# Optimization experiments

Hardware: AMD Instinct MI355X
Metric: run time of the kernel (lower is better)

Reference implementation:

```python
import jax, jax.numpy as jnp
import numpy as np

N, D, H, B, E = 100000, 256, 256, 128, 128
STEPS = 5


def setup_inputs() -> dict:
    key = jax.random.key(0)
    ks = jax.random.split(key, 16)
    w = lambda i, shape: (jax.random.normal(ks[i], shape, jnp.float32) * 0.05)
    inp = {
        "x": jax.random.normal(ks[0], (N, D), jnp.float32),
        "batch_idxs": jnp.sort(jax.random.randint(ks[1], (N,), 0, B)),
        # FNN: Linear(D,H) -> ELU -> Linear(H,H)
        "fnn_W1": w(2, (D, H)), "fnn_b1": jnp.zeros((H,), jnp.float32),
        "fnn_W2": w(3, (H, H)), "fnn_b2": jnp.zeros((H,), jnp.float32),
        # 3-layer LSTM, input 2H (layer 0) / H (layers 1,2), hidden H
        "Wih0": w(4, (4 * H, 2 * H)), "Whh0": w(5, (4 * H, H)),
        "bih0": jnp.zeros((4 * H,), jnp.float32), "bhh0": jnp.zeros((4 * H,), jnp.float32),
        "Wih1": w(6, (4 * H, H)), "Whh1": w(7, (4 * H, H)),
        "bih1": jnp.zeros((4 * H,), jnp.float32), "bhh1": jnp.zeros((4 * H,), jnp.float32),
        "Wih2": w(8, (4 * H, H)), "Whh2": w(9, (4 * H, H)),
        "bih2": jnp.zeros((4 * H,), jnp.float32), "bhh2": jnp.zeros((4 * H,), jnp.float32),
        # output Linear(2H, E)
        "out_W": w(10, (2 * H, E)), "out_b": jnp.zeros((E,), jnp.float32),
    }
    return inp


def _lstm_cell(xin, h, c, Wih, Whh, bih, bhh):
    gates = xin @ Wih.T + bih + h @ Whh.T + bhh  # (B, 4H)
    i, f, g, o = jnp.split(gates, 4, axis=-1)    # PyTorch gate order i,f,g,o
    c = jax.nn.sigmoid(f) * c + jax.nn.sigmoid(i) * jnp.tanh(g)
    h = jax.nn.sigmoid(o) * jnp.tanh(c)
    return h, c


def reference(x, batch_idxs, fnn_W1, fnn_b1, fnn_W2, fnn_b2,
              Wih0, Whh0, bih0, bhh0, Wih1, Whh1, bih1, bhh1,
              Wih2, Whh2, bih2, bhh2, out_W, out_b):
    # FNN (ELU between layers)
    hfeat = jax.nn.elu(x @ fnn_W1 + fnn_b1) @ fnn_W2 + fnn_b2  # (N, H)

    Wihs, Whhs = (Wih0, Wih1, Wih2), (Whh0, Whh1, Whh2)
    bihs, bhhs = (bih0, bih1, bih2), (bhh0, bhh1, bhh2)
    hs = [jnp.zeros((B, H), hfeat.dtype) for _ in range(3)]
    cs = [jnp.zeros((B, H), hfeat.dtype) for _ in range(3)]
    q_star = jnp.zeros((B, 2 * H), hfeat.dtype)

    for _ in range(STEPS):
        layer_in = q_star
        for l in range(3):
            hs[l], cs[l] = _lstm_cell(layer_in, hs[l], cs[l], Wihs[l], Whhs[l], bihs[l], bhhs[l])
            layer_in = hs[l]
        q = layer_in  # (B, H)
        # segment (per-graph) attention softmax over nodes
        e = jnp.sum(hfeat * q[batch_idxs], axis=-1)                     # (N,)
        m = jax.ops.segment_max(e, batch_idxs, num_segments=B)
        m = jnp.where(jnp.isfinite(m), m, 0.0)                          # guard empty segments
        ex = jnp.exp(e - m[batch_idxs])
        denom = jax.ops.segment_sum(ex, batch_idxs, num_segments=B) + 1e-16
        a = ex / denom[batch_idxs]                                      # (N,)
        r = jax.ops.segment_sum(a[:, None] * hfeat, batch_idxs, num_segments=B)  # (B, H)
        q_star = jnp.concatenate([q, r], axis=-1)                       # (B, 2H)

    return q_star @ out_W + out_b  # (B, E)
```

## Files before the change

kernel.cpp:

```cpp
#include <hip/hip_runtime.h>

#define NN 100000
#define NSTEP 5
#define LSTR 264

typedef unsigned short ushort_t;
typedef __attribute__((ext_vector_type(8))) short short8;
typedef __attribute__((ext_vector_type(4))) float floatx4;

__device__ __forceinline__ ushort_t f2bf(float f){
  union { float f; unsigned u; } v; v.f = f;
  unsigned r = v.u + 0x7fffu + ((v.u >> 16) & 1u);
  return (ushort_t)(r >> 16);
}
__device__ __forceinline__ float bf2f(ushort_t s){
  union { unsigned u; float f; } v; v.u = ((unsigned)s) << 16;
  return v.f;
}
__device__ __forceinline__ float sigf(float x){ return 1.0f/(1.0f+__expf(-x)); }

__global__ __launch_bounds__(512, 2) void fnn_fused(const float* __restrict__ x,
    const ushort_t* __restrict__ W1P, const float* __restrict__ b1,
    const ushort_t* __restrict__ W2P, const float* __restrict__ b2,
    ushort_t* __restrict__ hfeat)
{
  __shared__ ushort_t xbuf[2][32 * LSTR];
  __shared__ ushort_t tbuf[32 * LSTR];
  int tid = threadIdx.x;
  int w = tid >> 6, lane = tid & 63, qd = lane >> 4, r16 = lane & 15;

  short8 w1r[8][2], w2r[8][2];
  #pragma unroll
  for (int kc = 0; kc < 8; kc++)
    #pragma unroll
    for (int j = 0; j < 2; j++){
      size_t off = (size_t)(((w*2 + j)*8 + kc)*64 + lane)*8;
      w1r[kc][j] = *(const short8*)(W1P + off);
      w2r[kc][j] = *(const short8*)(W2P + off);
    }
  float bb1[2], bb2[2];
  #pragma unroll
  for (int j = 0; j < 2; j++){
    int col = w*32 + j*16 + r16;
    bb1[j] = b1[col];
    bb2[j] = b2[col];
  }

  size_t row0 = (size_t)blockIdx.x * 160;

  float4 xv[4];
  #pragma unroll
  for (int it = 0; it < 4; it++){
    int idx = it*512 + tid;
    xv[it] = *(const float4*)(x + (row0 + (idx>>6))*256 + (idx&63)*4);
  }
  #pragma unroll
  for (int it = 0; it < 4; it++){
    int idx = it*512 + tid;
    ushort4 pk = make_ushort4(f2bf(xv[it].x), f2bf(xv[it].y), f2bf(xv[it].z), f2bf(xv[it].w));
    *(ushort4*)&xbuf[0][(idx>>6)*LSTR + (idx&63)*4] = pk;
  }
  __syncthreads();

  int cur = 0;
  for (int t = 0; t < 5; t++){
    size_t rowt = row0 + t*32;
    if (t < 4){
      #pragma unroll
      for (int it = 0; it < 4; it++){
        int idx = it*512 + tid;
        xv[it] = *(const float4*)(x + (rowt + 32 + (idx>>6))*256 + (idx&63)*4);
      }
    }

    floatx4 acc[2][2];
    #pragma unroll
    for (int i=0;i<2;i++)
      #pragma unroll
      for (int j=0;j<2;j++) acc[i][j] = (floatx4){0.f,0.f,0.f,0.f};
    #pragma unroll
    for (int kc = 0; kc < 8; kc++){
      short8 af[2];
      #pragma unroll
      for (int i=0;i<2;i++)
        af[i] = *(const short8*)&xbuf[cur][(i*16 + r16)*LSTR + kc*32 + qd*8];
      #pragma unroll
      for (int i=0;i<2;i++)
        #pragma unroll
        for (int j=0;j<2;j++)
          acc[i][j] = __builtin_amdgcn_mfma_f32_16x16x32_bf16(af[i], w1r[kc][j], acc[i][j], 0, 0, 0);
    }

    #pragma unroll
    for (int i=0;i<2;i++){
      #pragma unroll
      for (int j=0;j<2;j++){
        int col = w*32 + j*16 + r16;
        #pragma unroll
        for (int rr=0;rr<4;rr++){
          int row = i*16 + qd*4 + rr;
          float v = acc[i][j][rr] + bb1[j];
          v = v > 0.f ? v : (__expf(v) - 1.0f);
          tbuf[row * LSTR + col] = f2bf(v);
        }
      }
    }
    __syncthreads();

    #pragma unroll
    for (int i=0;i<2;i++)
      #pragma unroll
      for (int j=0;j<2;j++) acc[i][j] = (floatx4){0.f,0.f,0.f,0.f};
    #pragma unroll
    for (int kc = 0; kc < 8; kc++){
      short8 af[2];
      #pragma unroll
      for (int i=0;i<2;i++)
        af[i] = *(const short8*)&tbuf[(i*16 + r16)*LSTR + kc*32 + qd*8];
      #pragma unroll
      for (int i=0;i<2;i++)
        #pragma unroll
        for (int j=0;j<2;j++)
          acc[i][j] = __builtin_amdgcn_mfma_f32_16x16x32_bf16(af[i], w2r[kc][j], acc[i][j], 0, 0, 0);
    }

    #pragma unroll
    for (int i=0;i<2;i++){
      #pragma unroll
      for (int j=0;j<2;j++){
        int col = w*32 + j*16 + r16;
        #pragma unroll
        for (int rr=0;rr<4;rr++){
          size_t row = rowt + i*16 + qd*4 + rr;
          hfeat[row * 256 + col] = f2bf(acc[i][j][rr] + bb2[j]);
        }
      }
    }

    if (t < 4){
      #pragma unroll
      for (int it = 0; it < 4; it++){
        int idx = it*512 + tid;
        ushort4 pk = make_ushort4(f2bf(xv[it].x), f2bf(xv[it].y), f2bf(xv[it].z), f2bf(xv[it].w));
        *(ushort4*)&xbuf[cur^1][(idx>>6)*LSTR + (idx&63)*4] = pk;
      }
    }
    __syncthreads();
    cur ^= 1;
  }
}

__global__ __launch_bounds__(256) void lstm_layer(const ushort_t* __restrict__ A, int lda,
    const ushort_t* __restrict__ WcP, const float* __restrict__ bcp, int KC,
    float* __restrict__ c, ushort_t* __restrict__ dstA, int sA,
    ushort_t* __restrict__ dstB, int sB, float* __restrict__ qdst)
{
  __shared__ float sbuf[3][4][256];
  int tid = threadIdx.x, w = tid >> 6, lane = tid & 63, qd = lane >> 4, r16 = lane & 15;
  int m0 = (blockIdx.x & 7) * 16, nt = blockIdx.x >> 3;
  int kcq = KC >> 2;
  int kc0 = w * kcq;

  floatx4 acc[4];
  #pragma unroll
  for (int g=0; g<4; g++) acc[g] = (floatx4){0.f,0.f,0.f,0.f};

  const ushort_t* Ar = A + (size_t)(m0 + r16) * lda + qd * 8;
  for (int kc = kc0; kc < kc0 + kcq; kc++){
    short8 av = *(const short8*)(Ar + kc*32);
    #pragma unroll
    for (int g = 0; g < 4; g++){
      short8 bv = *(const short8*)(WcP + (size_t)((((g*16 + nt)*KC) + kc)*64 + lane)*8);
      acc[g] = __builtin_amdgcn_mfma_f32_16x16x32_bf16(av, bv, acc[g], 0, 0, 0);
    }
  }
  if (w){
    #pragma unroll
    for (int g=0; g<4; g++) *(floatx4*)&sbuf[w-1][g][lane*4] = acc[g];
  }
  __syncthreads();
  if (w == 0){
    #pragma unroll
    for (int g=0; g<4; g++)
      #pragma unroll
      for (int t=0; t<3; t++){
        floatx4 p = *(floatx4*)&sbuf[t][g][lane*4];
        acc[g] = acc[g] + p;
      }
    int h = nt*16 + r16;
    float bci = bcp[h], bcf = bcp[256+h], bcg = bcp[512+h], bco = bcp[768+h];
    #pragma unroll
    for (int rr=0; rr<4; rr++){
      int row = m0 + qd*4 + rr;
      float gi = acc[0][rr] + bci;
      float gf = acc[1][rr] + bcf;
      float gg = acc[2][rr] + bcg;
      float go = acc[3][rr] + bco;
      float cp = c[row*256 + h];
      float cn = sigf(gf)*cp + sigf(gi)*tanhf(gg);
      float hn = sigf(go)*tanhf(cn);
      c[row*256 + h] = cn;
      ushort_t hb = f2bf(hn);
      dstA[row*sA + h] = hb;
      dstB[row*sB + h] = hb;
      if (qdst) qdst[row*512 + h] = hn;
    }
  }
}

__global__ __launch_bounds__(256) void attn_onepass(const ushort_t* __restrict__ hfeat,
    const int* __restrict__ seg, const float* __restrict__ q_star,
    float* __restrict__ r_part, float* __restrict__ z_part)
{
  __shared__ float sred[4][260];
  int b = blockIdx.x >> 3, p = blockIdx.x & 7;
  int w = threadIdx.x >> 6, lane = threadIdx.x & 63;
  int s0 = seg[b], s1 = seg[b+1], len = s1 - s0;
  int q0 = s0 + ((len * p) >> 3);
  int q1 = s0 + ((len * (p+1)) >> 3);

  float S0=0.f, S1=0.f, S2=0.f, S3=0.f, Z=0.f;

  int n = q0 + w;
  if (n < q1){
    float4 q = *(const float4*)(q_star + (size_t)b*512 + lane*4);
    #define LOADH(nn) (*(const ushort4*)(hfeat + (size_t)(nn)*256 + lane*4))
    ushort4 ha = LOADH(n);
    ushort4 hb = ha;
    if (n + 4 < q1) hb = LOADH(n + 4);
    for (; n < q1; n += 8){
      ushort4 hc = ha, hd = hb;
      if (n + 8  < q1) hc = LOADH(n + 8);
      if (n + 12 < q1) hd = LOADH(n + 12);
      float a0=bf2f(ha.x), a1=bf2f(ha.y), a2=bf2f(ha.z), a3=bf2f(ha.w);
      float da = a0*q.x + a1*q.y + a2*q.z + a3*q.w;
      float b0=0.f,b1=0.f,b2=0.f,b3=0.f, db=0.f;
      int vB = (n + 4) < q1;
      if (vB){
        b0=bf2f(hb.x); b1=bf2f(hb.y); b2=bf2f(hb.z); b3=bf2f(hb.w);
        db = b0*q.x + b1*q.y + b2*q.z + b3*q.w;
      }
      #pragma unroll
      for (int off = 32; off; off >>= 1){
        da += __shfl_xor(da, off);
        db += __shfl_xor(db, off);
      }
      float wa = __expf(da);
      Z += wa; S0 += wa*a0; S1 += wa*a1; S2 += wa*a2; S3 += wa*a3;
      if (vB){
        float wb = __expf(db);
        Z += wb; S0 += wb*b0; S1 += wb*b1; S2 += wb*b2; S3 += wb*b3;
      }
      ha = hc; hb = hd;
    }
    #undef LOADH
  }

  *(float4*)&sred[w][lane*4] = (float4){S0, S1, S2, S3};
  if (lane == 0) sred[w][256] = Z;
  __syncthreads();
  int f = threadIdx.x;
  if (f < 256){
    float v = sred[0][f] + sred[1][f] + sred[2][f] + sred[3][f];
    r_part[((size_t)p*128 + b)*256 + f] = v;
    if (f == 0)
      z_part[p*128 + b] = sred[0][256] + sred[1][256] + sred[2][256] + sred[3][256];
  }
}

__global__ __launch_bounds__(256) void attn_fin(const float* __restrict__ r_part,
    const float* __restrict__ z_part, float* __restrict__ q_star, ushort_t* __restrict__ xc0,
    const float* __restrict__ outW, const float* __restrict__ outb,
    float* __restrict__ out, int last)
{
  __shared__ float qs[512];
  int b = blockIdx.x, f = threadIdx.x;
  float s = 0.f, z = 0.f;
  #pragma unroll
  for (int t = 0; t < 8; t++){
    s += r_part[((size_t)(t*128 + b))*256 + f];
    z += z_part[t*128 + b];
  }
  float v = s / (z + 1e-16f);
  q_star[b*512 + 256 + f] = v;
  xc0[b*768 + 256 + f] = f2bf(v);
  if (last){
    qs[f] = q_star[b*512 + f];
    qs[256 + f] = v;
    __syncthreads();
    if (f < 128){
      float acc = outb[f];
      for (int k = 0; k < 512; k++) acc += qs[k] * outW[k*128 + f];
      out[b*128 + f] = acc;
    }
  }
}

__global__ void prep_all(const float* __restrict__ W1, const float* __restrict__ W2,
    const float* __restrict__ Wih0, const float* __restrict__ Whh0,
    const float* __restrict__ Wih1, const float* __restrict__ Whh1,
    const float* __restrict__ Wih2, const float* __restrict__ Whh2,
    const float* __restrict__ bih0, const float* __restrict__ bhh0,
    const float* __restrict__ bih1, const float* __restrict__ bhh1,
    const float* __restrict__ bih2, const float* __restrict__ bhh2,
    const int* __restrict__ bidx,
    ushort_t* __restrict__ W1P, ushort_t* __restrict__ W2P,
    ushort_t* __restrict__ Wc0P, ushort_t* __restrict__ Wc1P, ushort_t* __restrict__ Wc2P,
    float* __restrict__ c, ushort_t* __restrict__ xc, float* __restrict__ q_star,
    float* __restrict__ bc, int* __restrict__ seg)
{
  int i = blockIdx.x*256 + threadIdx.x;
  if (i < 131072){
    const float* W = (i < 65536) ? W1 : W2;
    ushort_t* P = (i < 65536) ? W1P : W2P;
    int r = i & 65535;
    int T = r >> 12, r2 = r & 4095;
    int kc = r2 >> 9, l = (r2 >> 3) & 63, j = r2 & 7;
    int k = kc*32 + ((l>>4)<<3) + j;
    int n = T*16 + (l & 15);
    P[r] = f2bf(W[k*256 + n]);
    return;
  }
  i -= 131072;
  if (i < 786432){
    int T = i / 12288, r2 = i - T*12288;
    int kc = r2 >> 9, l = (r2 >> 3) & 63, j = r2 & 7;
    int k = kc*32 + ((l>>4)<<3) + j;
    int g = T >> 4, n = (T & 15)*16 + (l & 15);
    int row = g*256 + n;
    Wc0P[i] = f2bf(k < 512 ? Wih0[row*512 + k] : Whh0[row*256 + (k - 512)]);
    return;
  }
  i -= 786432;
  if (i < 1048576){
    const float* Wih = (i < 524288) ? Wih1 : Wih2;
    const float* Whh = (i < 524288) ? Whh1 : Whh2;
    ushort_t* P = (i < 524288) ? Wc1P : Wc2P;
    int r = i & 524287;
    int T = r >> 13, r2 = r & 8191;
    int kc = r2 >> 9, l = (r2 >> 3) & 63, j = r2 & 7;
    int k = kc*32 + ((l>>4)<<3) + j;
    int g = T >> 4, n = (T & 15)*16 + (l & 15);
    int row = g*256 + n;
    P[r] = f2bf(k < 256 ? Wih[row*256 + k] : Whh[row*256 + (k - 256)]);
    return;
  }
  i -= 1048576;
  if (i < 98304) { c[i] = 0.f; return; }
  i -= 98304;
  if (i < 229376) { xc[i] = 0; return; }
  i -= 229376;
  if (i < 65536) { q_star[i] = 0.f; return; }
  i -= 65536;
  if (i < 3072) {
    int l = i >> 10, g = i & 1023;
    const float* bi = (l == 0) ? bih0 : ((l == 1) ? bih1 : bih2);
    const float* bh = (l == 0) ? bhh0 : ((l == 1) ? bhh1 : bhh2);
    bc[i] = bi[g] + bh[g];
    return;
  }
  i -= 3072;
  if (i < 129) {
    int lo = 0, hi = NN;
    while (lo < hi){ int mid = (lo + hi) >> 1; if (bidx[mid] < i) lo = mid + 1; else hi = mid; }
    seg[i] = lo;
    return;
  }
}

extern "C" void kernel_launch(void* const* d_in, const int* in_sizes, int n_in,
                              void* d_out, int out_size, void* d_ws, size_t ws_size,
                              hipStream_t stream)
{
  const float* x    = (const float*)d_in[0];
  const int*   bidx = (const int*)  d_in[1];
  const float* W1   = (const float*)d_in[2];
  const float* b1   = (const float*)d_in[3];
  const float* W2   = (const float*)d_in[4];
  const float* b2   = (const float*)d_in[5];
  const float* Wih0 = (const float*)d_in[6];
  const float* Whh0 = (const float*)d_in[7];
  const float* bih0 = (const float*)d_in[8];
  const float* bhh0 = (const float*)d_in[9];
  const float* Wih1 = (const float*)d_in[10];
  const float* Whh1 = (const float*)d_in[11];
  const float* bih1 = (const float*)d_in[12];
  const float* bhh1 = (const float*)d_in[13];
  const float* Wih2 = (const float*)d_in[14];
  const float* Whh2 = (const float*)d_in[15];
  const float* bih2 = (const float*)d_in[16];
  const float* bhh2 = (const float*)d_in[17];
  const float* outW = (const float*)d_in[18];
  const float* outb = (const float*)d_in[19];

  char* p = (char*)d_ws;
  auto alloc = [&](size_t bytes)->char*{ char* r = p; p += (bytes + 255) & ~(size_t)255; return r; };
  ushort_t* hfeat  = (ushort_t*)alloc((size_t)NN*256*2);
  ushort_t* W1P    = (ushort_t*)alloc(65536*2);
  ushort_t* W2P    = (ushort_t*)alloc(65536*2);
  ushort_t* Wc0P   = (ushort_t*)alloc(786432*2);
  ushort_t* Wc1P   = (ushort_t*)alloc(524288*2);
  ushort_t* Wc2P   = (ushort_t*)alloc(524288*2);
  float*    bc     = (float*)   alloc(3072*4);
  float*    c_all  = (float*)   alloc(98304*4);
  ushort_t* xc     = (ushort_t*)alloc(229376*2);
  float*    q_star = (float*)   alloc(65536*4);
  float*    r_part = (float*)   alloc(8*128*256*4);
  float*    z_part = (float*)   alloc(8*128*4);
  int*      seg    = (int*)     alloc(129*4);

  ushort_t* xc0 = xc;
  ushort_t* xc1 = xc + 98304;
  ushort_t* xc2 = xc + 163840;
  float* c0 = c_all, *c1 = c_all + 32768, *c2 = c_all + 65536;
  float* bc0 = bc, *bc1 = bc + 1024, *bc2 = bc + 2048;

  prep_all<<<9229, 256, 0, stream>>>(W1, W2, Wih0, Whh0, Wih1, Whh1, Wih2, Whh2,
                                     bih0, bhh0, bih1, bhh1, bih2, bhh2, bidx,
                                     W1P, W2P, Wc0P, Wc1P, Wc2P,
                                     c_all, xc, q_star, bc, seg);

  fnn_fused<<<625, 512, 0, stream>>>(x, W1P, b1, W2P, b2, hfeat);

  for (int s = 0; s < NSTEP; s++){
    lstm_layer<<<128, 256, 0, stream>>>(xc0, 768, Wc0P, bc0, 24, c0, xc0 + 512, 768, xc1, 512, nullptr);
    lstm_layer<<<128, 256, 0, stream>>>(xc1, 512, Wc1P, bc1, 16, c1, xc1 + 256, 512, xc2, 512, nullptr);
    lstm_layer<<<128, 256, 0, stream>>>(xc2, 512, Wc2P, bc2, 16, c2, xc2 + 256, 512, xc0, 768, q_star);
    attn_onepass<<<1024, 256, 0, stream>>>(hfeat, seg, q_star, r_part, z_part);
    attn_fin<<<128, 256, 0, stream>>>(r_part, z_part, q_star, xc0, outW, outb,
                                      (float*)d_out, s == NSTEP-1 ? 1 : 0);
  }
}
```

Before: 408.9 us.

## Stream FNN weights via LDS async loads and fuse attention finalize with last-block counter

The FNN kernel no longer holds both weight matrices in registers across a 160-row persistent loop. Each block now handles 32 rows and streams weight chunks into double-buffered LDS with global_load_lds, which frees registers and allows more, smaller blocks. Separately, attn_fin is merged into attn_onepass: a per-graph atomic counter picks the last partial block to do the reduction and write q_star, saving one launch per step. The cost is reloading the weights in every block and the overhead of the atomics and fences.

```diff
diff --git a/kernel.cpp b/kernel.cpp
--- a/kernel.cpp
+++ b/kernel.cpp
@@ -19,25 +19,20 @@
 }
 __device__ __forceinline__ float sigf(float x){ return 1.0f/(1.0f+__expf(-x)); }
 
-__global__ __launch_bounds__(512, 2) void fnn_fused(const float* __restrict__ x,
+__global__ __launch_bounds__(512) void fnn_fused(const float* __restrict__ x,
     const ushort_t* __restrict__ W1P, const float* __restrict__ b1,
     const ushort_t* __restrict__ W2P, const float* __restrict__ b2,
-    ushort_t* __restrict__ hfeat)
+    ushort_t* __restrict__ hfeat, int M)
 {
-  __shared__ ushort_t xbuf[2][32 * LSTR];
-  __shared__ ushort_t tbuf[32 * LSTR];
+  __shared__ ushort_t buf[32 * LSTR];
+  __shared__ ushort_t wst[2][8][2][512];
   int tid = threadIdx.x;
   int w = tid >> 6, lane = tid & 63, qd = lane >> 4, r16 = lane & 15;
-
-  short8 w1r[8][2], w2r[8][2];
-  #pragma unroll
-  for (int kc = 0; kc < 8; kc++)
-    #pragma unroll
-    for (int j = 0; j < 2; j++){
-      size_t off = (size_t)(((w*2 + j)*8 + kc)*64 + lane)*8;
-      w1r[kc][j] = *(const short8*)(W1P + off);
-      w2r[kc][j] = *(const short8*)(W2P + off);
-    }
+  size_t row0 = (size_t)blockIdx.x * 32;
+
+  typedef __attribute__((address_space(3))) unsigned int lds_u32;
+  typedef __attribute__((address_space(1))) const unsigned int glb_u32;
+
   float bb1[2], bb2[2];
   #pragma unroll
   for (int j = 0; j < 2; j++){
@@ -46,107 +41,97 @@
     bb2[j] = b2[col];
   }
 
-  size_t row0 = (size_t)blockIdx.x * 160;
-
-  float4 xv[4];
-  #pragma unroll
-  for (int it = 0; it < 4; it++){
-    int idx = it*512 + tid;
-    xv[it] = *(const float4*)(x + (row0 + (idx>>6))*256 + (idx&63)*4);
-  }
-  #pragma unroll
-  for (int it = 0; it < 4; it++){
-    int idx = it*512 + tid;
-    ushort4 pk = make_ushort4(f2bf(xv[it].x), f2bf(xv[it].y), f2bf(xv[it].z), f2bf(xv[it].w));
-    *(ushort4*)&xbuf[0][(idx>>6)*LSTR + (idx&63)*4] = pk;
-  }
-  __syncthreads();
-
-  int cur = 0;
-  for (int t = 0; t < 5; t++){
-    size_t rowt = row0 + t*32;
-    if (t < 4){
-      #pragma unroll
-      for (int it = 0; it < 4; it++){
-        int idx = it*512 + tid;
-        xv[it] = *(const float4*)(x + (rowt + 32 + (idx>>6))*256 + (idx&63)*4);
-      }
-    }
-
-    floatx4 acc[2][2];
+  {
+    float4 xv[4];
+    #pragma unroll
+    for (int it = 0; it < 4; it++){
+      int idx = it * 512 + tid;
+      xv[it] = *(const float4*)(x + (row0 + (idx >> 6)) * 256 + (idx & 63) * 4);
+    }
+    #pragma unroll
+    for (int it = 0; it < 4; it++){
+      int idx = it * 512 + tid;
+      ushort4 pk = make_ushort4(f2bf(xv[it].x), f2bf(xv[it].y), f2bf(xv[it].z), f2bf(xv[it].w));
+      *(ushort4*)&buf[(idx >> 6) * LSTR + (idx & 63) * 4] = pk;
+    }
+  }
+  __syncthreads();
+
+  auto STAGE = [&](const ushort_t* __restrict__ P, int kc, int ph){
+    #pragma unroll
+    for (int j = 0; j < 2; j++){
+      const ushort_t* gp = P + (size_t)(((w*2 + j)*8 + kc)*512) + lane*8;
+      __builtin_amdgcn_global_load_lds((glb_u32*)gp, (lds_u32*)&wst[ph][w][j][0], 16, 0, 0);
+    }
+  };
+
+  floatx4 acc[2][2];
+
+  auto GEMM = [&](const ushort_t* __restrict__ P, bool prestaged){
+    if (!prestaged){ STAGE(P, 0, 0); STAGE(P, 1, 1); }
     #pragma unroll
     for (int i=0;i<2;i++)
       #pragma unroll
       for (int j=0;j<2;j++) acc[i][j] = (floatx4){0.f,0.f,0.f,0.f};
     #pragma unroll
     for (int kc = 0; kc < 8; kc++){
-      short8 af[2];
+      int ph = kc & 1;
+      if (kc < 7) asm volatile("s_waitcnt vmcnt(2)" ::: "memory");
+      else        asm volatile("s_waitcnt vmcnt(0)" ::: "memory");
+      short8 af[2], bf[2];
       #pragma unroll
       for (int i=0;i<2;i++)
-        af[i] = *(const short8*)&xbuf[cur][(i*16 + r16)*LSTR + kc*32 + qd*8];
+        af[i] = *(const short8*)&buf[(i*16 + r16)*LSTR + kc*32 + qd*8];
+      #pragma unroll
+      for (int j=0;j<2;j++)
+        bf[j] = *(const short8*)&wst[ph][w][j][lane*8];
       #pragma unroll
       for (int i=0;i<2;i++)
         #pragma unroll
         for (int j=0;j<2;j++)
-          acc[i][j] = __builtin_amdgcn_mfma_f32_16x16x32_bf16(af[i], w1r[kc][j], acc[i][j], 0, 0, 0);
-    }
-
-    #pragma unroll
-    for (int i=0;i<2;i++){
-      #pragma unroll
-      for (int j=0;j<2;j++){
-        int col = w*32 + j*16 + r16;
-        #pragma unroll
-        for (int rr=0;rr<4;rr++){
-          int row = i*16 + qd*4 + rr;
-          float v = acc[i][j][rr] + bb1[j];
-          v = v > 0.f ? v : (__expf(v) - 1.0f);
-          tbuf[row * LSTR + col] = f2bf(v);
-        }
-      }
-    }
-    __syncthreads();
-
-    #pragma unroll
-    for (int i=0;i<2;i++)
-      #pragma unroll
-      for (int j=0;j<2;j++) acc[i][j] = (floatx4){0.f,0.f,0.f,0.f};
-    #pragma unroll
-    for (int kc = 0; kc < 8; kc++){
-      short8 af[2];
-      #pragma unroll
-      for (int i=0;i<2;i++)
-        af[i] = *(const short8*)&tbuf[(i*16 + r16)*LSTR + kc*32 + qd*8];
-      #pragma unroll
-      for (int i=0;i<2;i++)
-        #pragma unroll
-        for (int j=0;j<2;j++)
-          acc[i][j] = __builtin_amdgcn_mfma_f32_16x16x32_bf16(af[i], w2r[kc][j], acc[i][j], 0, 0, 0);
-    }
-
-    #pragma unroll
-    for (int i=0;i<2;i++){
-      #pragma unroll
-      for (int j=0;j<2;j++){
-        int col = w*32 + j*16 + r16;
-        #pragma unroll
-        for (int rr=0;rr<4;rr++){
-          size_t row = rowt + i*16 + qd*4 + rr;
-          hfeat[row * 256 + col] = f2bf(acc[i][j][rr] + bb2[j]);
-        }
-      }
-    }
-
-    if (t < 4){
-      #pragma unroll
-      for (int it = 0; it < 4; it++){
-        int idx = it*512 + tid;
-        ushort4 pk = make_ushort4(f2bf(xv[it].x), f2bf(xv[it].y), f2bf(xv[it].z), f2bf(xv[it].w));
-        *(ushort4*)&xbuf[cur^1][(idx>>6)*LSTR + (idx&63)*4] = pk;
-      }
-    }
-    __syncthreads();
-    cur ^= 1;
+          acc[i][j] = __builtin_amdgcn_mfma_f32_16x16x32_bf16(af[i], bf[j], acc[i][j], 0, 0, 0);
+      if (kc + 2 < 8){
+        asm volatile("s_waitcnt lgkmcnt(0)" ::: "memory");
+        STAGE(P, kc + 2, ph);
+      }
+    }
+  };
+
+  GEMM(W1P, false);
+
+  asm volatile("s_waitcnt lgkmcnt(0)" ::: "memory");
+  STAGE(W2P, 0, 0); STAGE(W2P, 1, 1);
+  __syncthreads();
+
+  #pragma unroll
+  for (int i=0;i<2;i++){
+    #pragma unroll
+    for (int j=0;j<2;j++){
+      int col = w*32 + j*16 + r16;
+      #pragma unroll
+      for (int rr=0;rr<4;rr++){
+        int row = i*16 + qd*4 + rr;
+        float v = acc[i][j][rr] + bb1[j];
+        v = v > 0.f ? v : (__expf(v) - 1.0f);
+        buf[row * LSTR + col] = f2bf(v);
+      }
+    }
+  }
+  __syncthreads();
+
+  GEMM(W2P, true);
+
+  #pragma unroll
+  for (int i=0;i<2;i++){
+    #pragma unroll
+    for (int j=0;j<2;j++){
+      int col = w*32 + j*16 + r16;
+      #pragma unroll
+      for (int rr=0;rr<4;rr++){
+        size_t row = row0 + i*16 + qd*4 + rr;
+        hfeat[row * 256 + col] = f2bf(acc[i][j][rr] + bb2[j]);
+      }
+    }
   }
 }
 
@@ -209,10 +194,15 @@
 }
 
 __global__ __launch_bounds__(256) void attn_onepass(const ushort_t* __restrict__ hfeat,
-    const int* __restrict__ seg, const float* __restrict__ q_star,
-    float* __restrict__ r_part, float* __restrict__ z_part)
+    const int* __restrict__ seg, float* __restrict__ q_star,
+    float* __restrict__ r_part, float* __restrict__ z_part,
+    ushort_t* __restrict__ xc0, const float* __restrict__ outW,
+    const float* __restrict__ outb, float* __restrict__ out,
+    unsigned int* __restrict__ cnt, int last)
 {
   __shared__ float sred[4][260];
+  __shared__ float qs[512];
+  __shared__ int lastb;
   int b = blockIdx.x >> 3, p = blockIdx.x & 7;
   int w = threadIdx.x >> 6, lane = threadIdx.x & 63;
   int s0 = seg[b], s1 = seg[b+1], len = s1 - s0;
@@ -260,21 +250,23 @@
   if (lane == 0) sred[w][256] = Z;
   __syncthreads();
   int f = threadIdx.x;
-  if (f < 256){
+  {
     float v = sred[0][f] + sred[1][f] + sred[2][f] + sred[3][f];
     r_part[((size_t)p*128 + b)*256 + f] = v;
     if (f == 0)
       z_part[p*128 + b] = sred[0][256] + sred[1][256] + sred[2][256] + sred[3][256];
   }
-}
-
-__global__ __launch_bounds__(256) void attn_fin(const float* __restrict__ r_part,
-    const float* __restrict__ z_part, float* __restrict__ q_star, ushort_t* __restrict__ xc0,
-    const float* __restrict__ outW, const float* __restrict__ outb,
-    float* __restrict__ out, int last)
-{
-  __shared__ float qs[512];
-  int b = blockIdx.x, f = threadIdx.x;
+
+  __threadfence();
+  __syncthreads();
+  if (f == 0){
+    unsigned int old = atomicAdd(&cnt[b], 1u);
+    lastb = (old == 7u);
+  }
+  __syncthreads();
+  if (!lastb) return;
+
+  __threadfence();
   float s = 0.f, z = 0.f;
   #pragma unroll
   for (int t = 0; t < 8; t++){
@@ -284,6 +276,7 @@
   float v = s / (z + 1e-16f);
   q_star[b*512 + 256 + f] = v;
   xc0[b*768 + 256 + f] = f2bf(v);
+  if (f == 0) atomicExch(&cnt[b], 0u);
   if (last){
     qs[f] = q_star[b*512 + f];
     qs[256 + f] = v;
@@ -307,7 +300,7 @@
     ushort_t* __restrict__ W1P, ushort_t* __restrict__ W2P,
     ushort_t* __restrict__ Wc0P, ushort_t* __restrict__ Wc1P, ushort_t* __restrict__ Wc2P,
     float* __restrict__ c, ushort_t* __restrict__ xc, float* __restrict__ q_star,
-    float* __restrict__ bc, int* __restrict__ seg)
+    float* __restrict__ bc, int* __restrict__ seg, unsigned int* __restrict__ cnt)
 {
   int i = blockIdx.x*256 + threadIdx.x;
   if (i < 131072){
@@ -366,6 +359,8 @@
     seg[i] = lo;
     return;
   }
+  i -= 129;
+  if (i < 128) cnt[i] = 0u;
 }
 
 extern "C" void kernel_launch(void* const* d_in, const int* in_sizes, int n_in,
@@ -408,6 +403,7 @@
   float*    r_part = (float*)   alloc(8*128*256*4);
   float*    z_part = (float*)   alloc(8*128*4);
   int*      seg    = (int*)     alloc(129*4);
+  unsigned int* cnt = (unsigned int*)alloc(128*4);
 
   ushort_t* xc0 = xc;
   ushort_t* xc1 = xc + 98304;
@@ -415,19 +411,19 @@
   float* c0 = c_all, *c1 = c_all + 32768, *c2 = c_all + 65536;
   float* bc0 = bc, *bc1 = bc + 1024, *bc2 = bc + 2048;
 
-  prep_all<<<9229, 256, 0, stream>>>(W1, W2, Wih0, Whh0, Wih1, Whh1, Wih2, Whh2,
+  prep_all<<<9230, 256, 0, stream>>>(W1, W2, Wih0, Whh0, Wih1, Whh1, Wih2, Whh2,
                                      bih0, bhh0, bih1, bhh1, bih2, bhh2, bidx,
                                      W1P, W2P, Wc0P, Wc1P, Wc2P,
-                                     c_all, xc, q_star, bc, seg);
-
-  fnn_fused<<<625, 512, 0, stream>>>(x, W1P, b1, W2P, b2, hfeat);
+                                     c_all, xc, q_star, bc, seg, cnt);
+
+  fnn_fused<<<3125, 512, 0, stream>>>(x, W1P, b1, W2P, b2, hfeat, NN);
 
   for (int s = 0; s < NSTEP; s++){
     lstm_layer<<<128, 256, 0, stream>>>(xc0, 768, Wc0P, bc0, 24, c0, xc0 + 512, 768, xc1, 512, nullptr);
     lstm_layer<<<128, 256, 0, stream>>>(xc1, 512, Wc1P, bc1, 16, c1, xc1 + 256, 512, xc2, 512, nullptr);
     lstm_layer<<<128, 256, 0, stream>>>(xc2, 512, Wc2P, bc2, 16, c2, xc2 + 256, 512, xc0, 768, q_star);
-    attn_onepass<<<1024, 256, 0, stream>>>(hfeat, seg, q_star, r_part, z_part);
-    attn_fin<<<128, 256, 0, stream>>>(r_part, z_part, q_star, xc0, outW, outb,
-                                      (float*)d_out, s == NSTEP-1 ? 1 : 0);
-  }
-}
+    attn_onepass<<<1024, 256, 0, stream>>>(hfeat, seg, q_star, r_part, z_part,
+                                           xc0, outW, outb, (float*)d_out, cnt,
+                                           s == NSTEP-1 ? 1 : 0);
+  }
+}
```

After: 914.1 us. +123.6%, slower.
